# Performance work log

Measured on AMD Instinct MI355X. Metric: run time of the kernel, lower is better.

The kernel has to match this reference:

```python
import jax, jax.numpy as jnp
import numpy as np

N_NODES = 100000
N_EDGES = 1600000
N_FEAT = 128
HID = 64


def setup_inputs() -> dict:
    key = jax.random.key(0)
    ks = jax.random.split(key, 8)
    s = 0.05
    return {
        "x": jax.random.normal(ks[0], (N_NODES, N_FEAT), jnp.float32),
        "edge_index": jax.random.randint(ks[1], (2, N_EDGES), 0, N_NODES, jnp.int64),
        "labels": jax.random.randint(ks[2], (N_NODES, 1), 0, 2, jnp.int32),
        "W1": jax.random.normal(ks[3], (N_FEAT, HID), jnp.float32) * s,
        "b1": jnp.zeros((HID,), jnp.float32),
        "W2": jax.random.normal(ks[4], (HID, HID), jnp.float32) * s,
        "b2": jnp.zeros((HID,), jnp.float32),
        "W3": jax.random.normal(ks[5], (HID, HID), jnp.float32) * s,
        "b3": jnp.zeros((HID,), jnp.float32),
        "lW1": jax.random.normal(ks[6], (HID, 8), jnp.float32) * s,
        "lb1": jnp.zeros((8,), jnp.float32),
        "lW2": jax.random.normal(ks[7], (8, 1), jnp.float32) * s,
        "lb2": jnp.zeros((1,), jnp.float32),
    }


def reference(x, edge_index, labels, W1, b1, W2, b2, W3, b3, lW1, lb1, lW2, lb2):
    n = x.shape[0]
    # PyG GCNConv: add self-loops, symmetric D^{-1/2}(A+I)D^{-1/2} normalization
    loop = jnp.arange(n)
    row = jnp.concatenate([edge_index[0], loop])  # sources
    col = jnp.concatenate([edge_index[1], loop])  # targets (aggregation)
    deg = jax.ops.segment_sum(jnp.ones(col.shape, x.dtype), col, num_segments=n)
    dinv = jax.lax.rsqrt(deg)  # deg >= 1 thanks to self loops
    norm = dinv[row] * dinv[col]  # [E+N]

    def gcn(h, W, b):
        m = (h @ W)[row] * norm[:, None]  # gather + scale per edge
        return jax.ops.segment_sum(m, col, num_segments=n) + b

    h = jax.nn.relu(gcn(x, W1, b1))   # dropout inactive in eval mode
    h = jax.nn.relu(gcn(h, W2, b2))
    h = jax.nn.relu(gcn(h, W3, b3))
    h = jax.nn.relu(h @ lW1 + lb1)
    p = jax.nn.sigmoid(h @ lW2 + lb2)  # [N,1]

    y = labels.astype(x.dtype)
    # generate_weights(labels): class-balance weights (minority class up-weighted)
    pm = jnp.mean(y)
    w = y * (1.0 - pm) + (1.0 - y) * pm
    eps = 1e-7
    pc = jnp.clip(p, eps, 1.0 - eps)
    bce = -(y * jnp.log(pc) + (1.0 - y) * jnp.log(1.0 - pc))
    loss = jnp.mean(w * bce)
    return loss, p
```

## Files before the change

kernel.cpp:

```cpp
#include <hip/hip_runtime.h>
#include <cstdint>
#include <cstddef>

typedef __attribute__((ext_vector_type(8))) short short8;
typedef __attribute__((ext_vector_type(4))) float f32x4;
typedef __attribute__((ext_vector_type(2))) float f32x2;

#define NBLK 512
#define NBLK_SHIFT 9

__device__ inline unsigned short f2bf(float f) {
  union { float f; unsigned int u; } x; x.f = f;
  unsigned int r = x.u + 0x7FFFu + ((x.u >> 16) & 1u);
  return (unsigned short)(r >> 16);
}
__device__ inline float bf2f(unsigned short s) {
  union { unsigned int u; float f; } x; x.u = ((unsigned int)s) << 16;
  return x.f;
}


__global__ __launch_bounds__(256) void hist_kernel(const int* __restrict__ cols,
                                                   int* __restrict__ histG,
                                                   const int* __restrict__ labels,
                                                   float* __restrict__ labelsum,
                                                   const float* __restrict__ W1,
                                                   const float* __restrict__ W2,
                                                   const float* __restrict__ W3,
                                                   unsigned short* __restrict__ Wt1,
                                                   unsigned short* __restrict__ Wt2,
                                                   unsigned short* __restrict__ Wt3,
                                                   int E, int N, int NBUCK) {
  __shared__ int h[512];
  if (blockIdx.x < 3) {
    const float* W; unsigned short* Wt; int K;
    if (blockIdx.x == 0)      { W = W1; Wt = Wt1; K = 128; }
    else if (blockIdx.x == 1) { W = W2; Wt = Wt2; K = 64; }
    else                      { W = W3; Wt = Wt3; K = 64; }
    int total = K * 64;
    for (int i = threadIdx.x; i < total; i += 256) {
      int n = i / K, k = i - n * K;
      Wt[i] = f2bf(W[k * 64 + n]);
    }
  }
  {
    int chunkL = (N + NBLK - 1) / NBLK;
    int ls = blockIdx.x * chunkL;
    int le = min(N, ls + chunkL);
    float v = 0.f;
    for (int i = ls + threadIdx.x; i < le; i += 256) v += (float)labels[i];
#pragma unroll
    for (int o = 32; o > 0; o >>= 1) v += __shfl_down(v, o);
    __shared__ float sl[4];
    if ((threadIdx.x & 63) == 0) sl[threadIdx.x >> 6] = v;
    __syncthreads();
    if (threadIdx.x == 0) labelsum[blockIdx.x] = sl[0] + sl[1] + sl[2] + sl[3];
  }
  for (int i = threadIdx.x; i < NBUCK; i += 256) h[i] = 0;
  __syncthreads();
  int chunk = (E + NBLK - 1) / NBLK;
  int s = blockIdx.x * chunk;
  int e = min(E, s + chunk);
  for (int i = s + threadIdx.x; i < e; i += 256) atomicAdd(&h[cols[i] >> 8], 1);
  __syncthreads();
  for (int i = threadIdx.x; i < NBUCK; i += 256)
    histG[blockIdx.x * NBUCK + i] = h[i];
}


__global__ __launch_bounds__(256) void scan_partials_t(const int* __restrict__ histG,
                                                       int* __restrict__ partials,
                                                       int total, int NBUCK) {
  int i = blockIdx.x * 256 + threadIdx.x;
  int v = 0;
  if (i < total) {
    int bucket = i >> NBLK_SHIFT, blk = i & (NBLK - 1);
    v = histG[blk * NBUCK + bucket];
  }
#pragma unroll
  for (int o = 32; o > 0; o >>= 1) v += __shfl_down(v, o);
  __shared__ int s[4];
  if ((threadIdx.x & 63) == 0) s[threadIdx.x >> 6] = v;
  __syncthreads();
  if (threadIdx.x == 0) partials[blockIdx.x] = s[0] + s[1] + s[2] + s[3];
}

__global__ __launch_bounds__(256) void scan_block(int* __restrict__ partials, int nb,
                                                  float* __restrict__ loss,
                                                  const float* __restrict__ labelsum,
                                                  float* __restrict__ pmsum) {
  __shared__ int tmp[256];
  __shared__ int carry;
  int tid = threadIdx.x;
  {
    float v = 0.f;
    for (int i = tid; i < NBLK; i += 256) v += labelsum[i];
#pragma unroll
    for (int o = 32; o > 0; o >>= 1) v += __shfl_down(v, o);
    __shared__ float sl[4];
    if ((tid & 63) == 0) sl[tid >> 6] = v;
    __syncthreads();
    if (tid == 0) *pmsum = sl[0] + sl[1] + sl[2] + sl[3];
  }
  if (tid == 0) { carry = 0; *loss = 0.f; }
  __syncthreads();
  for (int base = 0; base < nb; base += 256) {
    int i = base + tid;
    int v = (i < nb) ? partials[i] : 0;
    tmp[tid] = v;
    __syncthreads();
    int incl = v;
    for (int o = 1; o < 256; o <<= 1) {
      int t = (tid >= o) ? tmp[tid - o] : 0;
      __syncthreads();
      incl += t;
      tmp[tid] = incl;
      __syncthreads();
    }
    int total = tmp[255];
    int c = carry;
    if (i < nb) partials[i] = c + incl - v;
    __syncthreads();
    if (tid == 0) carry = c + total;
    __syncthreads();
  }
}

__global__ __launch_bounds__(256) void scan_final_t(const int* __restrict__ histG,
                                                    const int* __restrict__ partials,
                                                    int* __restrict__ scannedG,
                                                    int total, int NBUCK) {
  __shared__ int tmp[256];
  int tid = threadIdx.x;
  int i = blockIdx.x * 256 + tid;
  int bucket = i >> NBLK_SHIFT, blk = i & (NBLK - 1);
  int v = (i < total) ? histG[blk * NBUCK + bucket] : 0;
  tmp[tid] = v;
  __syncthreads();
  int incl = v;
  for (int o = 1; o < 256; o <<= 1) {
    int t = (tid >= o) ? tmp[tid - o] : 0;
    __syncthreads();
    incl += t;
    tmp[tid] = incl;
    __syncthreads();
  }
  if (i < total) scannedG[blk * NBUCK + bucket] = partials[blockIdx.x] + incl - v;
}


__global__ __launch_bounds__(256) void scatter_kernel(const int* __restrict__ rows,
                                                      const int* __restrict__ cols,
                                                      const int* __restrict__ scannedG,
                                                      unsigned int* __restrict__ packed,
                                                      int E, int NBUCK) {
  __shared__ int cur[512];
  for (int i = threadIdx.x; i < NBUCK; i += 256)
    cur[i] = scannedG[blockIdx.x * NBUCK + i];
  __syncthreads();
  int chunk = (E + NBLK - 1) / NBLK;
  int s = blockIdx.x * chunk;
  int e = min(E, s + chunk);
  for (int i = s + threadIdx.x; i < e; i += 256) {
    int c = cols[i];
    int r = rows[i];
    int pos = atomicAdd(&cur[c >> 8], 1);
    packed[pos] = ((unsigned int)(c & 255) << 24) | (unsigned int)r;
  }
}


__global__ __launch_bounds__(1024) void csr_finalize(const unsigned int* __restrict__ packed,
                                                     const int* __restrict__ scannedG,
                                                     int* __restrict__ sorted_src,
                                                     int* __restrict__ offsets,
                                                     float* __restrict__ dinv,
                                                     int N, int E, int NBUCK) {
  __shared__ int h[256];
  __shared__ int tmp[256];
  __shared__ int cur[256];
  int b = blockIdx.x;
  int tid = threadIdx.x;
  int base = scannedG[b];
  int end = (b + 1 < NBUCK) ? scannedG[b + 1] : E;
  if (tid < 256) h[tid] = 0;
  __syncthreads();
  for (int i = base + tid; i < end; i += 1024)
    atomicAdd(&h[packed[i] >> 24], 1);
  __syncthreads();
  if (tid < 256) {
    int v = h[tid];
    tmp[tid] = v;
  }
  __syncthreads();
  if (tid < 256) {
    int v = h[tid];
    int incl = v;
    for (int o = 1; o < 256; o <<= 1) {
      int t = (tid >= o) ? tmp[tid - o] : 0;
      __syncthreads();
      incl += t;
      tmp[tid] = incl;
      __syncthreads();
    }
    int excl = incl - v;
    int node = b * 256 + tid;
    if (node < N) {
      offsets[node] = base + excl;
      dinv[node] = rsqrtf((float)(v + 1));
    }
    cur[tid] = base + excl;
    if (b == NBUCK - 1 && tid == 0) offsets[N] = E;
  } else {
    for (int o = 1; o < 256; o <<= 1) { __syncthreads(); __syncthreads(); }
  }
  __syncthreads();
  for (int i = base + tid; i < end; i += 1024) {
    unsigned int p = packed[i];
    int pos = atomicAdd(&cur[p >> 24], 1);
    sorted_src[pos] = (int)(p & 0xFFFFFFu);
  }
}


template <int K, bool F32IN>
__global__ __launch_bounds__(256) void mfma_gemm(const void* __restrict__ hv,
                                                 const unsigned short* __restrict__ Wt,
                                                 const float* __restrict__ dinv,
                                                 unsigned char* __restrict__ out, int N) {
  __shared__ unsigned short tile[4][16 * 68];
  int w = threadIdx.x >> 6, lane = threadIdx.x & 63;
  int m = lane & 15, quad = lane >> 4;
  int m0 = blockIdx.x * 64 + w * 16;
  int rowA = m0 + m;
  bool rowOK = rowA < N;
  f32x4 acc[4] = {{0.f,0.f,0.f,0.f},{0.f,0.f,0.f,0.f},{0.f,0.f,0.f,0.f},{0.f,0.f,0.f,0.f}};
#pragma unroll
  for (int kc = 0; kc < K / 32; ++kc) {
    short8 a = {0, 0, 0, 0, 0, 0, 0, 0};
    if (rowOK) {
      if (F32IN) {
        const float* hp = (const float*)hv + (size_t)rowA * K + kc * 32 + quad * 8;
        float4 p0 = ((const float4*)hp)[0];
        float4 p1 = ((const float4*)hp)[1];
        a[0] = (short)f2bf(p0.x); a[1] = (short)f2bf(p0.y);
        a[2] = (short)f2bf(p0.z); a[3] = (short)f2bf(p0.w);
        a[4] = (short)f2bf(p1.x); a[5] = (short)f2bf(p1.y);
        a[6] = (short)f2bf(p1.z); a[7] = (short)f2bf(p1.w);
      } else {
        a = *(const short8*)((const unsigned short*)hv + (size_t)rowA * K + kc * 32 + quad * 8);
      }
    }
#pragma unroll
    for (int t = 0; t < 4; ++t) {
      short8 b = *(const short8*)(Wt + (size_t)(t * 16 + m) * K + kc * 32 + quad * 8);
      acc[t] = __builtin_amdgcn_mfma_f32_16x16x32_bf16(a, b, acc[t], 0, 0, 0);
    }
  }
  unsigned short* tw = tile[w];
#pragma unroll
  for (int r = 0; r < 4; ++r) {
    int row = quad * 4 + r;
    int gr = m0 + row;
    float dv = dinv[gr < N ? gr : 0];
#pragma unroll
    for (int t = 0; t < 4; ++t)
      tw[row * 68 + t * 16 + m] = f2bf(acc[t][r] * dv);
  }
#pragma unroll
  for (int p = 0; p < 4; ++p) {
    int row = p * 4 + (lane >> 4);
    int ch = lane & 15;
    int gr = m0 + row;
    if (gr < N) {
      uint2 v = *(const uint2*)(tw + row * 68 + ch * 4);
      float f0 = bf2f((unsigned short)(v.x & 0xFFFFu));
      float f1 = bf2f((unsigned short)(v.x >> 16));
      float f2 = bf2f((unsigned short)(v.y & 0xFFFFu));
      float f3 = bf2f((unsigned short)(v.y >> 16));
      int pk = 0;
      pk = __builtin_amdgcn_cvt_pk_fp8_f32(f0, f1, pk, false);
      pk = __builtin_amdgcn_cvt_pk_fp8_f32(f2, f3, pk, true);
      *(unsigned int*)(out + (size_t)gr * 64 + ch * 4) = (unsigned int)pk;
    }
  }
}


__global__ __launch_bounds__(256) void aggregate(const unsigned char* __restrict__ A8,
                                                 const int* __restrict__ offsets,
                                                 const int* __restrict__ sorted_src,
                                                 const float* __restrict__ dinv,
                                                 const float* __restrict__ bias,
                                                 unsigned short* __restrict__ out, int N) {
  int c = blockIdx.x * 32 + (threadIdx.x >> 3);
  if (c >= N) return;
  int l = threadIdx.x & 7;
  int obase = threadIdx.x & 56;
  int s = offsets[c], e = offsets[c + 1];
  float dc = dinv[c];
  uint2 svr = *(const uint2*)(A8 + ((size_t)c << 6) + l * 8);
  f32x2 a0 = {0.f, 0.f}, a1 = {0.f, 0.f}, a2 = {0.f, 0.f}, a3 = {0.f, 0.f};
  for (int base = s; base < e; base += 16) {
    int i0 = base + l, i1 = base + 8 + l;
    int r0 = (i0 < e) ? __builtin_nontemporal_load(sorted_src + i0) : 0;
    int r1 = (i1 < e) ? __builtin_nontemporal_load(sorted_src + i1) : 0;
    int cnt = e - base; if (cnt > 16) cnt = 16;
    int rj[16];
#pragma unroll
    for (int t = 0; t < 8; ++t)  rj[t] = __shfl(r0, obase + t);
#pragma unroll
    for (int t = 8; t < 16; ++t) rj[t] = __shfl(r1, obase + (t - 8));
#pragma unroll
    for (int t = 0; t < 16; ++t) {
      if (t < cnt) {
        uint2 v = *(const uint2*)(A8 + ((size_t)(unsigned int)rj[t] << 6) + l * 8);
        a0 += __builtin_amdgcn_cvt_pk_f32_fp8((int)v.x, false);
        a1 += __builtin_amdgcn_cvt_pk_f32_fp8((int)v.x, true);
        a2 += __builtin_amdgcn_cvt_pk_f32_fp8((int)v.y, false);
        a3 += __builtin_amdgcn_cvt_pk_f32_fp8((int)v.y, true);
      }
    }
  }
  f32x2 s0 = __builtin_amdgcn_cvt_pk_f32_fp8((int)svr.x, false);
  f32x2 s1 = __builtin_amdgcn_cvt_pk_f32_fp8((int)svr.x, true);
  f32x2 s2 = __builtin_amdgcn_cvt_pk_f32_fp8((int)svr.y, false);
  f32x2 s3 = __builtin_amdgcn_cvt_pk_f32_fp8((int)svr.y, true);
  float acc[8] = {a0[0] + s0[0], a0[1] + s0[1], a1[0] + s1[0], a1[1] + s1[1],
                  a2[0] + s2[0], a2[1] + s2[1], a3[0] + s3[0], a3[1] + s3[1]};
  const float* bp = bias + l * 8;
  short8 ov;
#pragma unroll
  for (int q = 0; q < 8; ++q) {
    float v = fmaf(acc[q], dc, bp[q]);
    ov[q] = (short)f2bf(v > 0.f ? v : 0.f);
  }
  *(short8*)(out + (size_t)c * 64 + l * 8) = ov;
}


__global__ __launch_bounds__(256) void head_loss_kernel(const unsigned short* __restrict__ h,
                                                        const float* __restrict__ lW1,
                                                        const float* __restrict__ lb1,
                                                        const float* __restrict__ lW2,
                                                        const float* __restrict__ lb2,
                                                        const int* __restrict__ labels,
                                                        const float* __restrict__ pmsum,
                                                        float* __restrict__ p,
                                                        float* __restrict__ loss, int N) {
  int n = blockIdx.x * 256 + threadIdx.x;
  float contrib = 0.f;
  if (n < N) {
    float acc[8];
#pragma unroll
    for (int j = 0; j < 8; ++j) acc[j] = lb1[j];
    const unsigned short* hr = h + (size_t)n * 64;
#pragma unroll
    for (int ch = 0; ch < 8; ++ch) {
      short8 hv8 = ((const short8*)hr)[ch];
#pragma unroll
      for (int q = 0; q < 8; ++q) {
        float v = bf2f((unsigned short)hv8[q]);
        int k = ch * 8 + q;
#pragma unroll
        for (int j = 0; j < 8; ++j) acc[j] = fmaf(v, lW1[k * 8 + j], acc[j]);
      }
    }
    float s = lb2[0];
#pragma unroll
    for (int j = 0; j < 8; ++j) {
      float a = acc[j] > 0.f ? acc[j] : 0.f;
      s = fmaf(a, lW2[j], s);
    }
    float pv = 1.0f / (1.0f + expf(-s));
    p[n] = pv;
    float pm = *pmsum / (float)N;
    float y = (float)labels[n];
    float w = y * (1.f - pm) + (1.f - y) * pm;
    float pc = fminf(fmaxf(pv, 1e-7f), 1.f - 1e-7f);
    float bce = -(y * logf(pc) + (1.f - y) * logf(1.f - pc));
    contrib = w * bce / (float)N;
  }
#pragma unroll
  for (int o = 32; o > 0; o >>= 1) contrib += __shfl_down(contrib, o);
  __shared__ float sh[4];
  int lane = threadIdx.x & 63, w = threadIdx.x >> 6;
  if (lane == 0) sh[w] = contrib;
  __syncthreads();
  if (threadIdx.x == 0) atomicAdd(loss, sh[0] + sh[1] + sh[2] + sh[3]);
}


extern "C" void kernel_launch(void* const* d_in, const int* in_sizes, int n_in,
                              void* d_out, int out_size, void* d_ws, size_t ws_size,
                              hipStream_t stream) {
  const float* x      = (const float*)d_in[0];
  const int*   ei     = (const int*)d_in[1];
  const int*   labels = (const int*)d_in[2];
  const float* W1 = (const float*)d_in[3];
  const float* b1 = (const float*)d_in[4];
  const float* W2 = (const float*)d_in[5];
  const float* b2 = (const float*)d_in[6];
  const float* W3 = (const float*)d_in[7];
  const float* b3 = (const float*)d_in[8];
  const float* lW1 = (const float*)d_in[9];
  const float* lb1 = (const float*)d_in[10];
  const float* lW2 = (const float*)d_in[11];
  const float* lb2 = (const float*)d_in[12];

  int N = in_sizes[2];
  int E = in_sizes[1] / 2;
  const int* rows = ei;
  const int* cols = ei + E;

  int nb = (N + 255) / 256;
  int Npad = (N + 63) & ~63;
  int NBUCK = (N + 255) >> 8;
  int totalH = NBUCK * NBLK;
  int nb2 = (totalH + 255) / 256;

  char* ws = (char*)d_ws;
  unsigned char*  A8  = (unsigned char*)ws;
  unsigned short* H   = (unsigned short*)(ws + (size_t)Npad * 64);
  unsigned short* Wt1 = H + (size_t)Npad * 64;
  unsigned short* Wt2 = Wt1 + 64 * 128;
  unsigned short* Wt3 = Wt2 + 64 * 64;
  float* dinv     = (float*)(Wt3 + 64 * 64);
  int*   offsets  = (int*)(dinv + N);
  int*   histG    = offsets + N + 1;
  int*   scanned  = histG + totalH;
  unsigned int* packed = (unsigned int*)(scanned + totalH);
  int*   sorted   = (int*)(packed + E);
  int*   partials = sorted + E;
  float* pmsum    = (float*)(partials + nb2);
  float* labelsum = pmsum + 1;

  float* loss = (float*)d_out;
  float* p    = (float*)d_out + 1;

  int gemmBlocks = Npad / 64;
  int aggBlocks  = (N + 31) / 32;

  hist_kernel<<<NBLK, 256, 0, stream>>>(cols, histG, labels, labelsum,
                                        W1, W2, W3, Wt1, Wt2, Wt3, E, N, NBUCK);
  scan_partials_t<<<nb2, 256, 0, stream>>>(histG, partials, totalH, NBUCK);
  scan_block<<<1, 256, 0, stream>>>(partials, nb2, loss, labelsum, pmsum);
  scan_final_t<<<nb2, 256, 0, stream>>>(histG, partials, scanned, totalH, NBUCK);
  scatter_kernel<<<NBLK, 256, 0, stream>>>(rows, cols, scanned, packed, E, NBUCK);
  csr_finalize<<<NBUCK, 1024, 0, stream>>>(packed, scanned, sorted, offsets, dinv, N, E, NBUCK);

  mfma_gemm<128, true><<<gemmBlocks, 256, 0, stream>>>(x, Wt1, dinv, A8, N);
  aggregate<<<aggBlocks, 256, 0, stream>>>(A8, offsets, sorted, dinv, b1, H, N);

  mfma_gemm<64, false><<<gemmBlocks, 256, 0, stream>>>(H, Wt2, dinv, A8, N);
  aggregate<<<aggBlocks, 256, 0, stream>>>(A8, offsets, sorted, dinv, b2, H, N);

  mfma_gemm<64, false><<<gemmBlocks, 256, 0, stream>>>(H, Wt3, dinv, A8, N);
  aggregate<<<aggBlocks, 256, 0, stream>>>(A8, offsets, sorted, dinv, b3, H, N);

  head_loss_kernel<<<nb, 256, 0, stream>>>(H, lW1, lb1, lW2, lb2, labels, pmsum, p, loss, N);
}
```

Baseline: 300.1 us.

## Fuse aggregation with next-layer GEMM and final aggregation with head/loss

Each GCN aggregation now computes the next layer's 64x64 MFMA GEMM in the same block, staging the aggregated bf16 rows in shared memory and writing fp8 output directly. The separate bf16 H buffer round-trip and two GEMM launches go away, and ping-pong A8 buffers replace the shared one. The last aggregation is fused with the MLP head and loss, reducing the 8-wide hidden layer across the 8 lanes of each node with shuffles. This removes intermediate global traffic and launches, at the cost of extra syncthreads and register pressure in the aggregation kernel.

```diff
diff --git a/kernel.cpp b/kernel.cpp
--- a/kernel.cpp
+++ b/kernel.cpp
@@ -223,11 +223,11 @@
 }
 
 
-template <int K, bool F32IN>
-__global__ __launch_bounds__(256) void mfma_gemm(const void* __restrict__ hv,
-                                                 const unsigned short* __restrict__ Wt,
-                                                 const float* __restrict__ dinv,
-                                                 unsigned char* __restrict__ out, int N) {
+__global__ __launch_bounds__(256) void mfma_gemm1(const float* __restrict__ xv,
+                                                  const unsigned short* __restrict__ Wt,
+                                                  const float* __restrict__ dinv,
+                                                  unsigned char* __restrict__ out, int N) {
+  const int K = 128;
   __shared__ unsigned short tile[4][16 * 68];
   int w = threadIdx.x >> 6, lane = threadIdx.x & 63;
   int m = lane & 15, quad = lane >> 4;
@@ -239,17 +239,13 @@
   for (int kc = 0; kc < K / 32; ++kc) {
     short8 a = {0, 0, 0, 0, 0, 0, 0, 0};
     if (rowOK) {
-      if (F32IN) {
-        const float* hp = (const float*)hv + (size_t)rowA * K + kc * 32 + quad * 8;
-        float4 p0 = ((const float4*)hp)[0];
-        float4 p1 = ((const float4*)hp)[1];
-        a[0] = (short)f2bf(p0.x); a[1] = (short)f2bf(p0.y);
-        a[2] = (short)f2bf(p0.z); a[3] = (short)f2bf(p0.w);
-        a[4] = (short)f2bf(p1.x); a[5] = (short)f2bf(p1.y);
-        a[6] = (short)f2bf(p1.z); a[7] = (short)f2bf(p1.w);
-      } else {
-        a = *(const short8*)((const unsigned short*)hv + (size_t)rowA * K + kc * 32 + quad * 8);
-      }
+      const float* hp = xv + (size_t)rowA * K + kc * 32 + quad * 8;
+      float4 p0 = ((const float4*)hp)[0];
+      float4 p1 = ((const float4*)hp)[1];
+      a[0] = (short)f2bf(p0.x); a[1] = (short)f2bf(p0.y);
+      a[2] = (short)f2bf(p0.z); a[3] = (short)f2bf(p0.w);
+      a[4] = (short)f2bf(p1.x); a[5] = (short)f2bf(p1.y);
+      a[6] = (short)f2bf(p1.z); a[7] = (short)f2bf(p1.w);
     }
 #pragma unroll
     for (int t = 0; t < 4; ++t) {
@@ -287,19 +283,27 @@
 }
 
 
-__global__ __launch_bounds__(256) void aggregate(const unsigned char* __restrict__ A8,
-                                                 const int* __restrict__ offsets,
-                                                 const int* __restrict__ sorted_src,
-                                                 const float* __restrict__ dinv,
-                                                 const float* __restrict__ bias,
-                                                 unsigned short* __restrict__ out, int N) {
-  int c = blockIdx.x * 32 + (threadIdx.x >> 3);
-  if (c >= N) return;
+__global__ __launch_bounds__(256) void agg_gemm(const unsigned char* __restrict__ A8in,
+                                                const int* __restrict__ offsets,
+                                                const int* __restrict__ sorted_src,
+                                                const float* __restrict__ dinv,
+                                                const float* __restrict__ bias,
+                                                const unsigned short* __restrict__ Wt,
+                                                unsigned char* __restrict__ A8out, int N) {
+  __shared__ unsigned short hl[32 * 68];
+  int cl = threadIdx.x >> 3;
+  int c = blockIdx.x * 32 + cl;
   int l = threadIdx.x & 7;
   int obase = threadIdx.x & 56;
-  int s = offsets[c], e = offsets[c + 1];
-  float dc = dinv[c];
-  uint2 svr = *(const uint2*)(A8 + ((size_t)c << 6) + l * 8);
+  bool ok = c < N;
+  int s = 0, e = 0;
+  float dc = 0.f;
+  uint2 svr = {0u, 0u};
+  if (ok) {
+    s = offsets[c]; e = offsets[c + 1];
+    dc = dinv[c];
+    svr = *(const uint2*)(A8in + ((size_t)c << 6) + l * 8);
+  }
   f32x2 a0 = {0.f, 0.f}, a1 = {0.f, 0.f}, a2 = {0.f, 0.f}, a3 = {0.f, 0.f};
   for (int base = s; base < e; base += 16) {
     int i0 = base + l, i1 = base + 8 + l;
@@ -314,7 +318,7 @@
 #pragma unroll
     for (int t = 0; t < 16; ++t) {
       if (t < cnt) {
-        uint2 v = *(const uint2*)(A8 + ((size_t)(unsigned int)rj[t] << 6) + l * 8);
+        uint2 v = *(const uint2*)(A8in + ((size_t)(unsigned int)rj[t] << 6) + l * 8);
         a0 += __builtin_amdgcn_cvt_pk_f32_fp8((int)v.x, false);
         a1 += __builtin_amdgcn_cvt_pk_f32_fp8((int)v.x, true);
         a2 += __builtin_amdgcn_cvt_pk_f32_fp8((int)v.y, false);
@@ -322,70 +326,177 @@
       }
     }
   }
-  f32x2 s0 = __builtin_amdgcn_cvt_pk_f32_fp8((int)svr.x, false);
-  f32x2 s1 = __builtin_amdgcn_cvt_pk_f32_fp8((int)svr.x, true);
-  f32x2 s2 = __builtin_amdgcn_cvt_pk_f32_fp8((int)svr.y, false);
-  f32x2 s3 = __builtin_amdgcn_cvt_pk_f32_fp8((int)svr.y, true);
-  float acc[8] = {a0[0] + s0[0], a0[1] + s0[1], a1[0] + s1[0], a1[1] + s1[1],
-                  a2[0] + s2[0], a2[1] + s2[1], a3[0] + s3[0], a3[1] + s3[1]};
-  const float* bp = bias + l * 8;
-  short8 ov;
-#pragma unroll
-  for (int q = 0; q < 8; ++q) {
-    float v = fmaf(acc[q], dc, bp[q]);
-    ov[q] = (short)f2bf(v > 0.f ? v : 0.f);
-  }
-  *(short8*)(out + (size_t)c * 64 + l * 8) = ov;
-}
-
-
-__global__ __launch_bounds__(256) void head_loss_kernel(const unsigned short* __restrict__ h,
-                                                        const float* __restrict__ lW1,
-                                                        const float* __restrict__ lb1,
-                                                        const float* __restrict__ lW2,
-                                                        const float* __restrict__ lb2,
-                                                        const int* __restrict__ labels,
-                                                        const float* __restrict__ pmsum,
-                                                        float* __restrict__ p,
-                                                        float* __restrict__ loss, int N) {
-  int n = blockIdx.x * 256 + threadIdx.x;
+  {
+    f32x2 s0 = __builtin_amdgcn_cvt_pk_f32_fp8((int)svr.x, false);
+    f32x2 s1 = __builtin_amdgcn_cvt_pk_f32_fp8((int)svr.x, true);
+    f32x2 s2 = __builtin_amdgcn_cvt_pk_f32_fp8((int)svr.y, false);
+    f32x2 s3 = __builtin_amdgcn_cvt_pk_f32_fp8((int)svr.y, true);
+    float acc[8] = {a0[0] + s0[0], a0[1] + s0[1], a1[0] + s1[0], a1[1] + s1[1],
+                    a2[0] + s2[0], a2[1] + s2[1], a3[0] + s3[0], a3[1] + s3[1]};
+    const float* bp = bias + l * 8;
+    unsigned int w0 = 0, w1 = 0, w2 = 0, w3 = 0;
+    if (ok) {
+      unsigned short hv[8];
+#pragma unroll
+      for (int q = 0; q < 8; ++q) {
+        float v = fmaf(acc[q], dc, bp[q]);
+        hv[q] = f2bf(v > 0.f ? v : 0.f);
+      }
+      w0 = (unsigned int)hv[0] | ((unsigned int)hv[1] << 16);
+      w1 = (unsigned int)hv[2] | ((unsigned int)hv[3] << 16);
+      w2 = (unsigned int)hv[4] | ((unsigned int)hv[5] << 16);
+      w3 = (unsigned int)hv[6] | ((unsigned int)hv[7] << 16);
+    }
+    unsigned int* dst = (unsigned int*)(hl + cl * 68 + l * 8);
+    dst[0] = w0; dst[1] = w1; dst[2] = w2; dst[3] = w3;
+  }
+  __syncthreads();
+  int wv = threadIdx.x >> 6, lane = threadIdx.x & 63;
+  int m = lane & 15, quad = lane >> 4;
+  int rbase = (wv & 1) * 16, cbase = (wv >> 1) * 32;
+  f32x4 acc2[2] = {{0.f,0.f,0.f,0.f},{0.f,0.f,0.f,0.f}};
+#pragma unroll
+  for (int kc = 0; kc < 2; ++kc) {
+    union { uint2 u[2]; short8 s8; } av;
+    const unsigned int* ap = (const unsigned int*)(hl + (rbase + m) * 68 + kc * 32 + quad * 8);
+    av.u[0] = ((const uint2*)ap)[0];
+    av.u[1] = ((const uint2*)ap)[1];
+#pragma unroll
+    for (int t = 0; t < 2; ++t) {
+      short8 b = *(const short8*)(Wt + (size_t)(cbase + t * 16 + m) * 64 + kc * 32 + quad * 8);
+      acc2[t] = __builtin_amdgcn_mfma_f32_16x16x32_bf16(av.s8, b, acc2[t], 0, 0, 0);
+    }
+  }
+  __syncthreads();
+#pragma unroll
+  for (int r = 0; r < 4; ++r) {
+    int row = rbase + quad * 4 + r;
+    int gr = blockIdx.x * 32 + row;
+    float dv = dinv[gr < N ? gr : 0];
+#pragma unroll
+    for (int t = 0; t < 2; ++t)
+      hl[row * 68 + cbase + t * 16 + m] = f2bf(acc2[t][r] * dv);
+  }
+  __syncthreads();
+#pragma unroll
+  for (int u = 0; u < 2; ++u) {
+    int id = threadIdx.x * 2 + u;
+    int row = id >> 4, ch = id & 15;
+    int gr = blockIdx.x * 32 + row;
+    if (gr < N) {
+      uint2 v = *(const uint2*)(hl + row * 68 + ch * 4);
+      float f0 = bf2f((unsigned short)(v.x & 0xFFFFu));
+      float f1 = bf2f((unsigned short)(v.x >> 16));
+      float f2 = bf2f((unsigned short)(v.y & 0xFFFFu));
+      float f3 = bf2f((unsigned short)(v.y >> 16));
+      int pk = 0;
+      pk = __builtin_amdgcn_cvt_pk_fp8_f32(f0, f1, pk, false);
+      pk = __builtin_amdgcn_cvt_pk_fp8_f32(f2, f3, pk, true);
+      *(unsigned int*)(A8out + (size_t)gr * 64 + ch * 4) = (unsigned int)pk;
+    }
+  }
+}
+
+
+__global__ __launch_bounds__(256) void agg_head(const unsigned char* __restrict__ A8in,
+                                                const int* __restrict__ offsets,
+                                                const int* __restrict__ sorted_src,
+                                                const float* __restrict__ dinv,
+                                                const float* __restrict__ bias,
+                                                const float* __restrict__ lW1,
+                                                const float* __restrict__ lb1,
+                                                const float* __restrict__ lW2,
+                                                const float* __restrict__ lb2,
+                                                const int* __restrict__ labels,
+                                                const float* __restrict__ pmsum,
+                                                float* __restrict__ p,
+                                                float* __restrict__ loss, int N) {
+  int cl = threadIdx.x >> 3;
+  int c = blockIdx.x * 32 + cl;
+  int l = threadIdx.x & 7;
+  int obase = threadIdx.x & 56;
+  bool ok = c < N;
+  int s = 0, e = 0;
+  float dc = 0.f;
+  uint2 svr = {0u, 0u};
+  if (ok) {
+    s = offsets[c]; e = offsets[c + 1];
+    dc = dinv[c];
+    svr = *(const uint2*)(A8in + ((size_t)c << 6) + l * 8);
+  }
+  f32x2 a0 = {0.f, 0.f}, a1 = {0.f, 0.f}, a2 = {0.f, 0.f}, a3 = {0.f, 0.f};
+  for (int base = s; base < e; base += 16) {
+    int i0 = base + l, i1 = base + 8 + l;
+    int r0 = (i0 < e) ? __builtin_nontemporal_load(sorted_src + i0) : 0;
+    int r1 = (i1 < e) ? __builtin_nontemporal_load(sorted_src + i1) : 0;
+    int cnt = e - base; if (cnt > 16) cnt = 16;
+    int rj[16];
+#pragma unroll
+    for (int t = 0; t < 8; ++t)  rj[t] = __shfl(r0, obase + t);
+#pragma unroll
+    for (int t = 8; t < 16; ++t) rj[t] = __shfl(r1, obase + (t - 8));
+#pragma unroll
+    for (int t = 0; t < 16; ++t) {
+      if (t < cnt) {
+        uint2 v = *(const uint2*)(A8in + ((size_t)(unsigned int)rj[t] << 6) + l * 8);
+        a0 += __builtin_amdgcn_cvt_pk_f32_fp8((int)v.x, false);
+        a1 += __builtin_amdgcn_cvt_pk_f32_fp8((int)v.x, true);
+        a2 += __builtin_amdgcn_cvt_pk_f32_fp8((int)v.y, false);
+        a3 += __builtin_amdgcn_cvt_pk_f32_fp8((int)v.y, true);
+      }
+    }
+  }
   float contrib = 0.f;
-  if (n < N) {
-    float acc[8];
-#pragma unroll
-    for (int j = 0; j < 8; ++j) acc[j] = lb1[j];
-    const unsigned short* hr = h + (size_t)n * 64;
-#pragma unroll
-    for (int ch = 0; ch < 8; ++ch) {
-      short8 hv8 = ((const short8*)hr)[ch];
-#pragma unroll
-      for (int q = 0; q < 8; ++q) {
-        float v = bf2f((unsigned short)hv8[q]);
-        int k = ch * 8 + q;
-#pragma unroll
-        for (int j = 0; j < 8; ++j) acc[j] = fmaf(v, lW1[k * 8 + j], acc[j]);
+  {
+    f32x2 s0 = __builtin_amdgcn_cvt_pk_f32_fp8((int)svr.x, false);
+    f32x2 s1 = __builtin_amdgcn_cvt_pk_f32_fp8((int)svr.x, true);
+    f32x2 s2 = __builtin_amdgcn_cvt_pk_f32_fp8((int)svr.y, false);
+    f32x2 s3 = __builtin_amdgcn_cvt_pk_f32_fp8((int)svr.y, true);
+    float acc[8] = {a0[0] + s0[0], a0[1] + s0[1], a1[0] + s1[0], a1[1] + s1[1],
+                    a2[0] + s2[0], a2[1] + s2[1], a3[0] + s3[0], a3[1] + s3[1]};
+    const float* bp = bias + l * 8;
+    float hq[8];
+#pragma unroll
+    for (int q = 0; q < 8; ++q) {
+      float v = fmaf(acc[q], dc, bp[q]);
+      hq[q] = v > 0.f ? v : 0.f;
+    }
+    float acc8[8] = {0.f,0.f,0.f,0.f,0.f,0.f,0.f,0.f};
+#pragma unroll
+    for (int q = 0; q < 8; ++q) {
+      int k = l * 8 + q;
+#pragma unroll
+      for (int j = 0; j < 8; ++j) acc8[j] = fmaf(hq[q], lW1[k * 8 + j], acc8[j]);
+    }
+#pragma unroll
+    for (int j = 0; j < 8; ++j) {
+      acc8[j] += __shfl_xor(acc8[j], 1);
+      acc8[j] += __shfl_xor(acc8[j], 2);
+      acc8[j] += __shfl_xor(acc8[j], 4);
+    }
+    if (ok && l == 0) {
+      float sv = lb2[0];
+#pragma unroll
+      for (int j = 0; j < 8; ++j) {
+        float a = acc8[j] + lb1[j];
+        a = a > 0.f ? a : 0.f;
+        sv = fmaf(a, lW2[j], sv);
       }
-    }
-    float s = lb2[0];
-#pragma unroll
-    for (int j = 0; j < 8; ++j) {
-      float a = acc[j] > 0.f ? acc[j] : 0.f;
-      s = fmaf(a, lW2[j], s);
-    }
-    float pv = 1.0f / (1.0f + expf(-s));
-    p[n] = pv;
-    float pm = *pmsum / (float)N;
-    float y = (float)labels[n];
-    float w = y * (1.f - pm) + (1.f - y) * pm;
-    float pc = fminf(fmaxf(pv, 1e-7f), 1.f - 1e-7f);
-    float bce = -(y * logf(pc) + (1.f - y) * logf(1.f - pc));
-    contrib = w * bce / (float)N;
+      float pv = 1.0f / (1.0f + expf(-sv));
+      p[c] = pv;
+      float pm = *pmsum / (float)N;
+      float y = (float)labels[c];
+      float w = y * (1.f - pm) + (1.f - y) * pm;
+      float pc = fminf(fmaxf(pv, 1e-7f), 1.f - 1e-7f);
+      float bce = -(y * logf(pc) + (1.f - y) * logf(1.f - pc));
+      contrib = w * bce / (float)N;
+    }
   }
 #pragma unroll
   for (int o = 32; o > 0; o >>= 1) contrib += __shfl_down(contrib, o);
   __shared__ float sh[4];
-  int lane = threadIdx.x & 63, w = threadIdx.x >> 6;
-  if (lane == 0) sh[w] = contrib;
+  int lane = threadIdx.x & 63, wv = threadIdx.x >> 6;
+  if (lane == 0) sh[wv] = contrib;
   __syncthreads();
   if (threadIdx.x == 0) atomicAdd(loss, sh[0] + sh[1] + sh[2] + sh[3]);
 }
@@ -413,16 +524,15 @@
   const int* rows = ei;
   const int* cols = ei + E;
 
-  int nb = (N + 255) / 256;
   int Npad = (N + 63) & ~63;
   int NBUCK = (N + 255) >> 8;
   int totalH = NBUCK * NBLK;
   int nb2 = (totalH + 255) / 256;
 
   char* ws = (char*)d_ws;
-  unsigned char*  A8  = (unsigned char*)ws;
-  unsigned short* H   = (unsigned short*)(ws + (size_t)Npad * 64);
-  unsigned short* Wt1 = H + (size_t)Npad * 64;
+  unsigned char*  A8a = (unsigned char*)ws;
+  unsigned char*  A8b = (unsigned char*)(ws + (size_t)Npad * 64);
+  unsigned short* Wt1 = (unsigned short*)(ws + (size_t)Npad * 192);
   unsigned short* Wt2 = Wt1 + 64 * 128;
   unsigned short* Wt3 = Wt2 + 64 * 64;
   float* dinv     = (float*)(Wt3 + 64 * 64);
@@ -449,14 +559,10 @@
   scatter_kernel<<<NBLK, 256, 0, stream>>>(rows, cols, scanned, packed, E, NBUCK);
   csr_finalize<<<NBUCK, 1024, 0, stream>>>(packed, scanned, sorted, offsets, dinv, N, E, NBUCK);
 
-  mfma_gemm<128, true><<<gemmBlocks, 256, 0, stream>>>(x, Wt1, dinv, A8, N);
-  aggregate<<<aggBlocks, 256, 0, stream>>>(A8, offsets, sorted, dinv, b1, H, N);
-
-  mfma_gemm<64, false><<<gemmBlocks, 256, 0, stream>>>(H, Wt2, dinv, A8, N);
-  aggregate<<<aggBlocks, 256, 0, stream>>>(A8, offsets, sorted, dinv, b2, H, N);
-
-  mfma_gemm<64, false><<<gemmBlocks, 256, 0, stream>>>(H, Wt3, dinv, A8, N);
-  aggregate<<<aggBlocks, 256, 0, stream>>>(A8, offsets, sorted, dinv, b3, H, N);
-
-  head_loss_kernel<<<nb, 256, 0, stream>>>(H, lW1, lb1, lW2, lb2, labels, pmsum, p, loss, N);
-}
+  mfma_gemm1<<<gemmBlocks, 256, 0, stream>>>(x, Wt1, dinv, A8a, N);
+
+  agg_gemm<<<aggBlocks, 256, 0, stream>>>(A8a, offsets, sorted, dinv, b1, Wt2, A8b, N);
+  agg_gemm<<<aggBlocks, 256, 0, stream>>>(A8b, offsets, sorted, dinv, b2, Wt3, A8a, N);
+  agg_head<<<aggBlocks, 256, 0, stream>>>(A8a, offsets, sorted, dinv, b3,
+                                          lW1, lb1, lW2, lb2, labels, pmsum, p, loss, N);
+}
```

New measurement: 329.0 us. 9.6% more time.

## Split features into 8-byte planes for cache-local gather aggregation and fuse first GEMM

Applied to the files above, without the earlier changes.

Stores the FP8 projected features and bf16 hidden states as eight feature planes of 8 columns each. Aggregation runs per plane, so each gather pass touches a small, cache-resident array instead of full 64-byte rows. The first GEMM is fused into the CSR finalize kernel, and padded edge slots read a zeroed row instead of branching. Histogram and scatter blocks are also remapped to interleave chunks across XCDs. The cost is eight times more aggregation blocks that re-read the edge lists, plus shuffle reductions.

```diff
diff --git a/kernel.cpp b/kernel.cpp
--- a/kernel.cpp
+++ b/kernel.cpp
@@ -8,6 +8,8 @@
 
 #define NBLK 512
 #define NBLK_SHIFT 9
+
+__device__ inline int chunk_of_block(int bid) { return ((bid & 7) << 6) | (bid >> 3); }
 
 __device__ inline unsigned short f2bf(float f) {
   union { float f; unsigned int u; } x; x.f = f;
@@ -30,6 +32,8 @@
                                                    unsigned short* __restrict__ Wt1,
                                                    unsigned short* __restrict__ Wt2,
                                                    unsigned short* __restrict__ Wt3,
+                                                   unsigned char* __restrict__ zbase,
+                                                   size_t PS8,
                                                    int E, int N, int NBUCK) {
   __shared__ int h[512];
   if (blockIdx.x < 3) {
@@ -42,6 +46,8 @@
       int n = i / K, k = i - n * K;
       Wt[i] = f2bf(W[k * 64 + n]);
     }
+  } else if (blockIdx.x == 3 && threadIdx.x < 8) {
+    *(unsigned long long*)(zbase + (size_t)threadIdx.x * PS8) = 0ull;
   }
   {
     int chunkL = (N + NBLK - 1) / NBLK;
@@ -58,13 +64,14 @@
   }
   for (int i = threadIdx.x; i < NBUCK; i += 256) h[i] = 0;
   __syncthreads();
+  int cchunk = chunk_of_block(blockIdx.x);
   int chunk = (E + NBLK - 1) / NBLK;
-  int s = blockIdx.x * chunk;
+  int s = cchunk * chunk;
   int e = min(E, s + chunk);
   for (int i = s + threadIdx.x; i < e; i += 256) atomicAdd(&h[cols[i] >> 8], 1);
   __syncthreads();
   for (int i = threadIdx.x; i < NBUCK; i += 256)
-    histG[blockIdx.x * NBUCK + i] = h[i];
+    histG[cchunk * NBUCK + i] = h[i];
 }
 
 
@@ -155,11 +162,12 @@
                                                       unsigned int* __restrict__ packed,
                                                       int E, int NBUCK) {
   __shared__ int cur[512];
+  int cchunk = chunk_of_block(blockIdx.x);
   for (int i = threadIdx.x; i < NBUCK; i += 256)
-    cur[i] = scannedG[blockIdx.x * NBUCK + i];
+    cur[i] = scannedG[cchunk * NBUCK + i];
   __syncthreads();
   int chunk = (E + NBLK - 1) / NBLK;
-  int s = blockIdx.x * chunk;
+  int s = cchunk * chunk;
   int e = min(E, s + chunk);
   for (int i = s + threadIdx.x; i < e; i += 256) {
     int c = cols[i];
@@ -170,15 +178,20 @@
 }
 
 
-__global__ __launch_bounds__(1024) void csr_finalize(const unsigned int* __restrict__ packed,
-                                                     const int* __restrict__ scannedG,
-                                                     int* __restrict__ sorted_src,
-                                                     int* __restrict__ offsets,
-                                                     float* __restrict__ dinv,
-                                                     int N, int E, int NBUCK) {
+__global__ __launch_bounds__(1024) void csr_finalize_gemm1(const unsigned int* __restrict__ packed,
+                                                           const int* __restrict__ scannedG,
+                                                           int* __restrict__ sorted_src,
+                                                           int* __restrict__ offsets,
+                                                           float* __restrict__ dinv,
+                                                           const float* __restrict__ xv,
+                                                           const unsigned short* __restrict__ Wt,
+                                                           unsigned char* __restrict__ A8out,
+                                                           int N, int E, int NBUCK, size_t PS8) {
   __shared__ int h[256];
   __shared__ int tmp[256];
   __shared__ int cur[256];
+  __shared__ float sdinv[256];
+  __shared__ unsigned short gtile[16][16 * 72];
   int b = blockIdx.x;
   int tid = threadIdx.x;
   int base = scannedG[b];
@@ -205,10 +218,12 @@
     }
     int excl = incl - v;
     int node = b * 256 + tid;
+    float dv = rsqrtf((float)(v + 1));
     if (node < N) {
       offsets[node] = base + excl;
-      dinv[node] = rsqrtf((float)(v + 1));
-    }
+      dinv[node] = dv;
+    }
+    sdinv[tid] = dv;
     cur[tid] = base + excl;
     if (b == NBUCK - 1 && tid == 0) offsets[N] = E;
   } else {
@@ -220,126 +235,206 @@
     int pos = atomicAdd(&cur[p >> 24], 1);
     sorted_src[pos] = (int)(p & 0xFFFFFFu);
   }
-}
-
-
-template <int K, bool F32IN>
-__global__ __launch_bounds__(256) void mfma_gemm(const void* __restrict__ hv,
-                                                 const unsigned short* __restrict__ Wt,
-                                                 const float* __restrict__ dinv,
-                                                 unsigned char* __restrict__ out, int N) {
-  __shared__ unsigned short tile[4][16 * 68];
-  int w = threadIdx.x >> 6, lane = threadIdx.x & 63;
-  int m = lane & 15, quad = lane >> 4;
-  int m0 = blockIdx.x * 64 + w * 16;
-  int rowA = m0 + m;
-  bool rowOK = rowA < N;
-  f32x4 acc[4] = {{0.f,0.f,0.f,0.f},{0.f,0.f,0.f,0.f},{0.f,0.f,0.f,0.f},{0.f,0.f,0.f,0.f}};
-#pragma unroll
-  for (int kc = 0; kc < K / 32; ++kc) {
-    short8 a = {0, 0, 0, 0, 0, 0, 0, 0};
-    if (rowOK) {
-      if (F32IN) {
-        const float* hp = (const float*)hv + (size_t)rowA * K + kc * 32 + quad * 8;
+  {
+    const int K = 128;
+    int wv = tid >> 6;
+    int lane = tid & 63;
+    int m = lane & 15, quad = lane >> 4;
+    int lrow0 = wv * 16;
+    int m0 = b * 256 + lrow0;
+    int rowA = m0 + m;
+    bool rowOK = rowA < N;
+    f32x4 acc[4] = {{0.f,0.f,0.f,0.f},{0.f,0.f,0.f,0.f},{0.f,0.f,0.f,0.f},{0.f,0.f,0.f,0.f}};
+#pragma unroll
+    for (int kc = 0; kc < K / 32; ++kc) {
+      short8 a = {0, 0, 0, 0, 0, 0, 0, 0};
+      if (rowOK) {
+        const float* hp = xv + (size_t)rowA * K + kc * 32 + quad * 8;
         float4 p0 = ((const float4*)hp)[0];
         float4 p1 = ((const float4*)hp)[1];
         a[0] = (short)f2bf(p0.x); a[1] = (short)f2bf(p0.y);
         a[2] = (short)f2bf(p0.z); a[3] = (short)f2bf(p0.w);
         a[4] = (short)f2bf(p1.x); a[5] = (short)f2bf(p1.y);
         a[6] = (short)f2bf(p1.z); a[7] = (short)f2bf(p1.w);
-      } else {
-        a = *(const short8*)((const unsigned short*)hv + (size_t)rowA * K + kc * 32 + quad * 8);
       }
-    }
-#pragma unroll
-    for (int t = 0; t < 4; ++t) {
-      short8 b = *(const short8*)(Wt + (size_t)(t * 16 + m) * K + kc * 32 + quad * 8);
-      acc[t] = __builtin_amdgcn_mfma_f32_16x16x32_bf16(a, b, acc[t], 0, 0, 0);
-    }
-  }
-  unsigned short* tw = tile[w];
-#pragma unroll
-  for (int r = 0; r < 4; ++r) {
-    int row = quad * 4 + r;
-    int gr = m0 + row;
-    float dv = dinv[gr < N ? gr : 0];
-#pragma unroll
-    for (int t = 0; t < 4; ++t)
-      tw[row * 68 + t * 16 + m] = f2bf(acc[t][r] * dv);
-  }
-#pragma unroll
-  for (int p = 0; p < 4; ++p) {
-    int row = p * 4 + (lane >> 4);
-    int ch = lane & 15;
-    int gr = m0 + row;
+#pragma unroll
+      for (int t = 0; t < 4; ++t) {
+        short8 bb = *(const short8*)(Wt + (size_t)(t * 16 + m) * K + kc * 32 + quad * 8);
+        acc[t] = __builtin_amdgcn_mfma_f32_16x16x32_bf16(a, bb, acc[t], 0, 0, 0);
+      }
+    }
+    unsigned short* tw = gtile[wv];
+#pragma unroll
+    for (int r = 0; r < 4; ++r) {
+      int row = quad * 4 + r;
+      float dv = sdinv[lrow0 + row];
+#pragma unroll
+      for (int t = 0; t < 4; ++t)
+        tw[row * 72 + t * 16 + m] = f2bf(acc[t][r] * dv);
+    }
+  }
+  __syncthreads();
+#pragma unroll
+  for (int u = 0; u < 2; ++u) {
+    int id = u * 1024 + tid;
+    int plane = id >> 8, row = id & 255;
+    int gr = b * 256 + row;
     if (gr < N) {
-      uint2 v = *(const uint2*)(tw + row * 68 + ch * 4);
-      float f0 = bf2f((unsigned short)(v.x & 0xFFFFu));
-      float f1 = bf2f((unsigned short)(v.x >> 16));
-      float f2 = bf2f((unsigned short)(v.y & 0xFFFFu));
-      float f3 = bf2f((unsigned short)(v.y >> 16));
-      int pk = 0;
-      pk = __builtin_amdgcn_cvt_pk_fp8_f32(f0, f1, pk, false);
-      pk = __builtin_amdgcn_cvt_pk_fp8_f32(f2, f3, pk, true);
-      *(unsigned int*)(out + (size_t)gr * 64 + ch * 4) = (unsigned int)pk;
-    }
-  }
-}
-
-
-__global__ __launch_bounds__(256) void aggregate(const unsigned char* __restrict__ A8,
+      const unsigned int* s4 = (const unsigned int*)(gtile[row >> 4] + (row & 15) * 72 + plane * 8);
+      float f0 = bf2f((unsigned short)(s4[0] & 0xFFFFu));
+      float f1 = bf2f((unsigned short)(s4[0] >> 16));
+      float f2 = bf2f((unsigned short)(s4[1] & 0xFFFFu));
+      float f3 = bf2f((unsigned short)(s4[1] >> 16));
+      float f4 = bf2f((unsigned short)(s4[2] & 0xFFFFu));
+      float f5 = bf2f((unsigned short)(s4[2] >> 16));
+      float f6 = bf2f((unsigned short)(s4[3] & 0xFFFFu));
+      float f7 = bf2f((unsigned short)(s4[3] >> 16));
+      int pk0 = 0, pk1 = 0;
+      pk0 = __builtin_amdgcn_cvt_pk_fp8_f32(f0, f1, pk0, false);
+      pk0 = __builtin_amdgcn_cvt_pk_fp8_f32(f2, f3, pk0, true);
+      pk1 = __builtin_amdgcn_cvt_pk_fp8_f32(f4, f5, pk1, false);
+      pk1 = __builtin_amdgcn_cvt_pk_fp8_f32(f6, f7, pk1, true);
+      uint2 o; o.x = (unsigned int)pk0; o.y = (unsigned int)pk1;
+      *(uint2*)(A8out + (size_t)plane * PS8 + (size_t)gr * 8) = o;
+    }
+  }
+}
+
+
+__global__ __launch_bounds__(256) void agg_plane(const unsigned char* __restrict__ A8,
                                                  const int* __restrict__ offsets,
                                                  const int* __restrict__ sorted_src,
                                                  const float* __restrict__ dinv,
                                                  const float* __restrict__ bias,
-                                                 unsigned short* __restrict__ out, int N) {
-  int c = blockIdx.x * 32 + (threadIdx.x >> 3);
+                                                 unsigned short* __restrict__ Hp,
+                                                 int N, int ZR, size_t PS8, size_t PSHe) {
+  int p = blockIdx.x & 7;
+  int chunk = blockIdx.x >> 3;
+  int lane = threadIdx.x & 63;
+  int cl = threadIdx.x >> 2;
+  int c = chunk * 64 + cl;
   if (c >= N) return;
-  int l = threadIdx.x & 7;
-  int obase = threadIdx.x & 56;
+  int l4 = lane & 3;
+  const unsigned char* P = A8 + (size_t)p * PS8;
   int s = offsets[c], e = offsets[c + 1];
   float dc = dinv[c];
-  uint2 svr = *(const uint2*)(A8 + ((size_t)c << 6) + l * 8);
+  uint2 svr = *(const uint2*)(P + (size_t)c * 8);
   f32x2 a0 = {0.f, 0.f}, a1 = {0.f, 0.f}, a2 = {0.f, 0.f}, a3 = {0.f, 0.f};
   for (int base = s; base < e; base += 16) {
-    int i0 = base + l, i1 = base + 8 + l;
-    int r0 = (i0 < e) ? __builtin_nontemporal_load(sorted_src + i0) : 0;
-    int r1 = (i1 < e) ? __builtin_nontemporal_load(sorted_src + i1) : 0;
-    int cnt = e - base; if (cnt > 16) cnt = 16;
-    int rj[16];
-#pragma unroll
-    for (int t = 0; t < 8; ++t)  rj[t] = __shfl(r0, obase + t);
-#pragma unroll
-    for (int t = 8; t < 16; ++t) rj[t] = __shfl(r1, obase + (t - 8));
-#pragma unroll
-    for (int t = 0; t < 16; ++t) {
-      if (t < cnt) {
-        uint2 v = *(const uint2*)(A8 + ((size_t)(unsigned int)rj[t] << 6) + l * 8);
-        a0 += __builtin_amdgcn_cvt_pk_f32_fp8((int)v.x, false);
-        a1 += __builtin_amdgcn_cvt_pk_f32_fp8((int)v.x, true);
-        a2 += __builtin_amdgcn_cvt_pk_f32_fp8((int)v.y, false);
-        a3 += __builtin_amdgcn_cvt_pk_f32_fp8((int)v.y, true);
-      }
-    }
-  }
-  f32x2 s0 = __builtin_amdgcn_cvt_pk_f32_fp8((int)svr.x, false);
-  f32x2 s1 = __builtin_amdgcn_cvt_pk_f32_fp8((int)svr.x, true);
-  f32x2 s2 = __builtin_amdgcn_cvt_pk_f32_fp8((int)svr.y, false);
-  f32x2 s3 = __builtin_amdgcn_cvt_pk_f32_fp8((int)svr.y, true);
-  float acc[8] = {a0[0] + s0[0], a0[1] + s0[1], a1[0] + s1[0], a1[1] + s1[1],
-                  a2[0] + s2[0], a2[1] + s2[1], a3[0] + s3[0], a3[1] + s3[1]};
-  const float* bp = bias + l * 8;
-  short8 ov;
+    int i0 = base + l4 * 4;
+    int r0 = (i0     < e) ? sorted_src[i0]     : ZR;
+    int r1 = (i0 + 1 < e) ? sorted_src[i0 + 1] : ZR;
+    int r2 = (i0 + 2 < e) ? sorted_src[i0 + 2] : ZR;
+    int r3 = (i0 + 3 < e) ? sorted_src[i0 + 3] : ZR;
+    uint2 v0 = *(const uint2*)(P + (size_t)(unsigned int)r0 * 8);
+    uint2 v1 = *(const uint2*)(P + (size_t)(unsigned int)r1 * 8);
+    uint2 v2 = *(const uint2*)(P + (size_t)(unsigned int)r2 * 8);
+    uint2 v3 = *(const uint2*)(P + (size_t)(unsigned int)r3 * 8);
+    __builtin_amdgcn_sched_barrier(0);
+    a0 += __builtin_amdgcn_cvt_pk_f32_fp8((int)v0.x, false);
+    a1 += __builtin_amdgcn_cvt_pk_f32_fp8((int)v0.x, true);
+    a2 += __builtin_amdgcn_cvt_pk_f32_fp8((int)v0.y, false);
+    a3 += __builtin_amdgcn_cvt_pk_f32_fp8((int)v0.y, true);
+    a0 += __builtin_amdgcn_cvt_pk_f32_fp8((int)v1.x, false);
+    a1 += __builtin_amdgcn_cvt_pk_f32_fp8((int)v1.x, true);
+    a2 += __builtin_amdgcn_cvt_pk_f32_fp8((int)v1.y, false);
+    a3 += __builtin_amdgcn_cvt_pk_f32_fp8((int)v1.y, true);
+    a0 += __builtin_amdgcn_cvt_pk_f32_fp8((int)v2.x, false);
+    a1 += __builtin_amdgcn_cvt_pk_f32_fp8((int)v2.x, true);
+    a2 += __builtin_amdgcn_cvt_pk_f32_fp8((int)v2.y, false);
+    a3 += __builtin_amdgcn_cvt_pk_f32_fp8((int)v2.y, true);
+    a0 += __builtin_amdgcn_cvt_pk_f32_fp8((int)v3.x, false);
+    a1 += __builtin_amdgcn_cvt_pk_f32_fp8((int)v3.x, true);
+    a2 += __builtin_amdgcn_cvt_pk_f32_fp8((int)v3.y, false);
+    a3 += __builtin_amdgcn_cvt_pk_f32_fp8((int)v3.y, true);
+  }
+  float acc[8] = {a0[0], a0[1], a1[0], a1[1], a2[0], a2[1], a3[0], a3[1]};
 #pragma unroll
   for (int q = 0; q < 8; ++q) {
-    float v = fmaf(acc[q], dc, bp[q]);
-    ov[q] = (short)f2bf(v > 0.f ? v : 0.f);
-  }
-  *(short8*)(out + (size_t)c * 64 + l * 8) = ov;
-}
-
-
-__global__ __launch_bounds__(256) void head_loss_kernel(const unsigned short* __restrict__ h,
+    acc[q] += __shfl_xor(acc[q], 1);
+    acc[q] += __shfl_xor(acc[q], 2);
+  }
+  if (l4 == 0) {
+    f32x2 s0 = __builtin_amdgcn_cvt_pk_f32_fp8((int)svr.x, false);
+    f32x2 s1 = __builtin_amdgcn_cvt_pk_f32_fp8((int)svr.x, true);
+    f32x2 s2 = __builtin_amdgcn_cvt_pk_f32_fp8((int)svr.y, false);
+    f32x2 s3 = __builtin_amdgcn_cvt_pk_f32_fp8((int)svr.y, true);
+    acc[0] += s0[0]; acc[1] += s0[1]; acc[2] += s1[0]; acc[3] += s1[1];
+    acc[4] += s2[0]; acc[5] += s2[1]; acc[6] += s3[0]; acc[7] += s3[1];
+    const float* bp = bias + p * 8;
+    short8 ov;
+#pragma unroll
+    for (int q = 0; q < 8; ++q) {
+      float v = fmaf(acc[q], dc, bp[q]);
+      ov[q] = (short)f2bf(v > 0.f ? v : 0.f);
+    }
+    *(short8*)(Hp + (size_t)p * PSHe + (size_t)c * 8) = ov;
+  }
+}
+
+
+__global__ __launch_bounds__(256) void gemm_mid(const unsigned short* __restrict__ Hp,
+                                                const unsigned short* __restrict__ Wt,
+                                                const float* __restrict__ dinv,
+                                                unsigned char* __restrict__ A8out,
+                                                int N, size_t PSHe, size_t PS8) {
+  __shared__ unsigned short hl[64 * 72];
+  int lane = threadIdx.x & 63, wv = threadIdx.x >> 6;
+  int m = lane & 15, quad = lane >> 4;
+  int rbase = wv * 16;
+  int m0 = blockIdx.x * 64;
+  int rowA = m0 + rbase + m;
+  bool rowOK = rowA < N;
+  f32x4 acc[4] = {{0.f,0.f,0.f,0.f},{0.f,0.f,0.f,0.f},{0.f,0.f,0.f,0.f},{0.f,0.f,0.f,0.f}};
+#pragma unroll
+  for (int kc = 0; kc < 2; ++kc) {
+    short8 a = {0, 0, 0, 0, 0, 0, 0, 0};
+    if (rowOK)
+      a = *(const short8*)(Hp + (size_t)(kc * 4 + quad) * PSHe + (size_t)rowA * 8);
+#pragma unroll
+    for (int t = 0; t < 4; ++t) {
+      short8 b = *(const short8*)(Wt + (size_t)(t * 16 + m) * 64 + kc * 32 + quad * 8);
+      acc[t] = __builtin_amdgcn_mfma_f32_16x16x32_bf16(a, b, acc[t], 0, 0, 0);
+    }
+  }
+#pragma unroll
+  for (int r = 0; r < 4; ++r) {
+    int row = rbase + quad * 4 + r;
+    int gr = m0 + row;
+    float dv = dinv[gr < N ? gr : 0];
+#pragma unroll
+    for (int t = 0; t < 4; ++t)
+      hl[row * 72 + t * 16 + m] = f2bf(acc[t][r] * dv);
+  }
+  __syncthreads();
+#pragma unroll
+  for (int u = 0; u < 2; ++u) {
+    int id = u * 256 + threadIdx.x;
+    int plane = id >> 6, row = id & 63;
+    int gr = m0 + row;
+    if (gr < N) {
+      const unsigned int* s4 = (const unsigned int*)(hl + row * 72 + plane * 8);
+      float f0 = bf2f((unsigned short)(s4[0] & 0xFFFFu));
+      float f1 = bf2f((unsigned short)(s4[0] >> 16));
+      float f2 = bf2f((unsigned short)(s4[1] & 0xFFFFu));
+      float f3 = bf2f((unsigned short)(s4[1] >> 16));
+      float f4 = bf2f((unsigned short)(s4[2] & 0xFFFFu));
+      float f5 = bf2f((unsigned short)(s4[2] >> 16));
+      float f6 = bf2f((unsigned short)(s4[3] & 0xFFFFu));
+      float f7 = bf2f((unsigned short)(s4[3] >> 16));
+      int pk0 = 0, pk1 = 0;
+      pk0 = __builtin_amdgcn_cvt_pk_fp8_f32(f0, f1, pk0, false);
+      pk0 = __builtin_amdgcn_cvt_pk_fp8_f32(f2, f3, pk0, true);
+      pk1 = __builtin_amdgcn_cvt_pk_fp8_f32(f4, f5, pk1, false);
+      pk1 = __builtin_amdgcn_cvt_pk_fp8_f32(f6, f7, pk1, true);
+      uint2 o; o.x = (unsigned int)pk0; o.y = (unsigned int)pk1;
+      *(uint2*)(A8out + (size_t)plane * PS8 + (size_t)gr * 8) = o;
+    }
+  }
+}
+
+
+__global__ __launch_bounds__(256) void head_loss_kernel(const unsigned short* __restrict__ Hp,
                                                         const float* __restrict__ lW1,
                                                         const float* __restrict__ lb1,
                                                         const float* __restrict__ lW2,
@@ -347,17 +442,17 @@
                                                         const int* __restrict__ labels,
                                                         const float* __restrict__ pmsum,
                                                         float* __restrict__ p,
-                                                        float* __restrict__ loss, int N) {
+                                                        float* __restrict__ loss,
+                                                        int N, size_t PSHe) {
   int n = blockIdx.x * 256 + threadIdx.x;
   float contrib = 0.f;
   if (n < N) {
     float acc[8];
 #pragma unroll
     for (int j = 0; j < 8; ++j) acc[j] = lb1[j];
-    const unsigned short* hr = h + (size_t)n * 64;
 #pragma unroll
     for (int ch = 0; ch < 8; ++ch) {
-      short8 hv8 = ((const short8*)hr)[ch];
+      short8 hv8 = *(const short8*)(Hp + (size_t)ch * PSHe + (size_t)n * 8);
 #pragma unroll
       for (int q = 0; q < 8; ++q) {
         float v = bf2f((unsigned short)hv8[q]);
@@ -384,8 +479,8 @@
 #pragma unroll
   for (int o = 32; o > 0; o >>= 1) contrib += __shfl_down(contrib, o);
   __shared__ float sh[4];
-  int lane = threadIdx.x & 63, w = threadIdx.x >> 6;
-  if (lane == 0) sh[w] = contrib;
+  int lane = threadIdx.x & 63, wv = threadIdx.x >> 6;
+  if (lane == 0) sh[wv] = contrib;
   __syncthreads();
   if (threadIdx.x == 0) atomicAdd(loss, sh[0] + sh[1] + sh[2] + sh[3]);
 }
@@ -413,16 +508,20 @@
   const int* rows = ei;
   const int* cols = ei + E;
 
-  int nb = (N + 255) / 256;
   int Npad = (N + 63) & ~63;
+  int NpadZ = Npad + 32;
   int NBUCK = (N + 255) >> 8;
   int totalH = NBUCK * NBLK;
   int nb2 = (totalH + 255) / 256;
+  int nb = (N + 255) / 256;
+
+  size_t PS8  = (size_t)NpadZ * 8;
+  size_t PSHe = (size_t)Npad * 8;
 
   char* ws = (char*)d_ws;
   unsigned char*  A8  = (unsigned char*)ws;
-  unsigned short* H   = (unsigned short*)(ws + (size_t)Npad * 64);
-  unsigned short* Wt1 = H + (size_t)Npad * 64;
+  unsigned short* H   = (unsigned short*)(ws + 8 * PS8);
+  unsigned short* Wt1 = H + 8 * PSHe;
   unsigned short* Wt2 = Wt1 + 64 * 128;
   unsigned short* Wt3 = Wt2 + 64 * 64;
   float* dinv     = (float*)(Wt3 + 64 * 64);
@@ -438,25 +537,25 @@
   float* loss = (float*)d_out;
   float* p    = (float*)d_out + 1;
 
-  int gemmBlocks = Npad / 64;
-  int aggBlocks  = (N + 31) / 32;
+  int nch64   = (N + 63) / 64;
+  int aggGrid = nch64 * 8;
+  int ZR = Npad;
 
   hist_kernel<<<NBLK, 256, 0, stream>>>(cols, histG, labels, labelsum,
-                                        W1, W2, W3, Wt1, Wt2, Wt3, E, N, NBUCK);
+                                        W1, W2, W3, Wt1, Wt2, Wt3,
+                                        A8 + (size_t)Npad * 8, PS8, E, N, NBUCK);
   scan_partials_t<<<nb2, 256, 0, stream>>>(histG, partials, totalH, NBUCK);
   scan_block<<<1, 256, 0, stream>>>(partials, nb2, loss, labelsum, pmsum);
   scan_final_t<<<nb2, 256, 0, stream>>>(histG, partials, scanned, totalH, NBUCK);
   scatter_kernel<<<NBLK, 256, 0, stream>>>(rows, cols, scanned, packed, E, NBUCK);
-  csr_finalize<<<NBUCK, 1024, 0, stream>>>(packed, scanned, sorted, offsets, dinv, N, E, NBUCK);
-
-  mfma_gemm<128, true><<<gemmBlocks, 256, 0, stream>>>(x, Wt1, dinv, A8, N);
-  aggregate<<<aggBlocks, 256, 0, stream>>>(A8, offsets, sorted, dinv, b1, H, N);
-
-  mfma_gemm<64, false><<<gemmBlocks, 256, 0, stream>>>(H, Wt2, dinv, A8, N);
-  aggregate<<<aggBlocks, 256, 0, stream>>>(A8, offsets, sorted, dinv, b2, H, N);
-
-  mfma_gemm<64, false><<<gemmBlocks, 256, 0, stream>>>(H, Wt3, dinv, A8, N);
-  aggregate<<<aggBlocks, 256, 0, stream>>>(A8, offsets, sorted, dinv, b3, H, N);
-
-  head_loss_kernel<<<nb, 256, 0, stream>>>(H, lW1, lb1, lW2, lb2, labels, pmsum, p, loss, N);
-}
+
+  csr_finalize_gemm1<<<NBUCK, 1024, 0, stream>>>(packed, scanned, sorted, offsets, dinv,
+                                                 x, Wt1, A8, N, E, NBUCK, PS8);
+
+  agg_plane<<<aggGrid, 256, 0, stream>>>(A8, offsets, sorted, dinv, b1, H, N, ZR, PS8, PSHe);
+  gemm_mid<<<nch64, 256, 0, stream>>>(H, Wt2, dinv, A8, N, PSHe, PS8);
+  agg_plane<<<aggGrid, 256, 0, stream>>>(A8, offsets, sorted, dinv, b2, H, N, ZR, PS8, PSHe);
+  gemm_mid<<<nch64, 256, 0, stream>>>(H, Wt3, dinv, A8, N, PSHe, PS8);
+  agg_plane<<<aggGrid, 256, 0, stream>>>(A8, offsets, sorted, dinv, b3, H, N, ZR, PS8, PSHe);
+  head_loss_kernel<<<nb, 256, 0, stream>>>(H, lW1, lb1, lW2, lb2, labels, pmsum, p, loss, N, PSHe);
+}
```

Result: slower. 396.5 us (+32.1%).
